# Kernel tuning notes

Measured on AMD Instinct MI355X. Metric: run time of the kernel, lower is better.

The kernel has to match this reference:

```python
import jax, jax.numpy as jnp
import numpy as np

LENGTH = 4096
BATCH = 4096
N_OBS = 2


def setup_inputs() -> dict:
    key = jax.random.key(0)
    k1, k2, k3 = jax.random.split(key, 3)
    # Scale potentials down: the original chain performs no message
    # normalization, so we keep per-step log-growth tiny to avoid overflow.
    j = jax.random.normal(k1, (), dtype=jnp.float32) * 0.01
    b = jax.random.normal(k2, (N_OBS,), dtype=jnp.float32) * 0.01
    observations = jax.random.randint(k3, (BATCH, LENGTH), 0, N_OBS, dtype=jnp.int32)
    return {"j": j, "b": b, "observations": observations}


def reference(j, b, observations):
    # Max-product belief propagation on a binary-state chain CRF,
    # vectorized over the batch and scanned over the chain length.
    B, L = observations.shape
    values = jnp.array([-0.5, 0.5], dtype=jnp.float32)          # states {0,1} - 0.5
    pairs = values[:, None] * values[None, :]                    # [2,2] outer product
    psi = jnp.exp(j * pairs)                                     # [2,2] pairwise potential
    # Unary potentials phi[b_idx, i, s] = exp(b[obs] * values[s])
    phi = jnp.exp(b[observations][..., None] * values)           # [B,L,2]
    phi_tm = jnp.transpose(phi, (1, 0, 2))                       # time-major [L,B,2]

    def step(msg, phi_t):
        # msg_new[k] = max_l phi_t[l] * msg[l] * psi[k,l]
        x = phi_t * msg                                          # [B,2]
        new = jnp.max(x[:, None, :] * psi[None, :, :], axis=2)   # [B,2]
        return new, new

    ones = jnp.ones((B, 2), dtype=phi.dtype)
    # Forward messages: column 0 is ones, column t uses obs[0..t-1]
    _, fwd_msgs = jax.lax.scan(step, ones, phi_tm[:-1])          # [L-1,B,2]
    forward = jnp.concatenate([ones[None], fwd_msgs], axis=0)    # [L,B,2]
    # Backward messages: iterate i = L-1 .. 1, last column is ones
    _, bwd_msgs = jax.lax.scan(step, ones, phi_tm[1:][::-1])     # [L-1,B,2]
    backward = jnp.concatenate([bwd_msgs[::-1], ones[None]], axis=0)  # [L,B,2]

    beliefs = phi_tm * forward * backward                        # [L,B,2]
    return jnp.transpose(beliefs, (1, 2, 0))                     # [B,2,L]
```

## Files before the change

### kernel.cpp

```cpp
#include <hip/hip_runtime.h>
#include <hip/hip_bf16.h>
#include <math.h>

#define LENGTH 4096
#define BATCH  4096
#define CHUNK  8
#define NTHR   512
#define NWAVE  (NTHR / 64)

typedef float vf4 __attribute__((ext_vector_type(4)));

__device__ __forceinline__ void mp_compose(
    float a00, float a01, float a10, float a11,
    float b00, float b01, float b10, float b11,
    float& d00, float& d01, float& d10, float& d11) {
  d00 = fmaxf(a00 + b00, a01 + b10);
  d01 = fmaxf(a00 + b01, a01 + b11);
  d10 = fmaxf(a10 + b00, a11 + b10);
  d11 = fmaxf(a10 + b01, a11 + b11);
}

__device__ __forceinline__ void mp_step(
    float& f00, float& f01, float& f10, float& f11, float ui, float q) {
  float a0l0 = f00 - ui, a1l0 = f10 + ui;
  float a0l1 = f01 - ui, a1l1 = f11 + ui;
  float n00 = fmaxf(a0l0 + q, a1l0 - q);
  float n10 = fmaxf(a0l0 - q, a1l0 + q);
  float n01 = fmaxf(a0l1 + q, a1l1 - q);
  float n11 = fmaxf(a0l1 - q, a1l1 + q);
  f00 = n00; f01 = n01; f10 = n10; f11 = n11;
}

__global__ __launch_bounds__(NTHR, 8) void chain_bp_kernel(
    const float* __restrict__ jp, const float* __restrict__ bp,
    const int* __restrict__ obs, float* __restrict__ out) {
  const int row  = blockIdx.x;
  const int tid  = threadIdx.x;
  const int lane = tid & 63;
  const int wv   = tid >> 6;

  const float j  = jp[0];
  const float q  = 0.25f * j;
  const float u0 = 0.5f * bp[0];
  const float u1 = 0.5f * bp[1];
  const float wb = -fabsf(q);

  const int t0 = tid * CHUNK;
  const int4* op = reinterpret_cast<const int4*>(obs + (size_t)row * LENGTH + t0);
  float u[CHUNK];
#pragma unroll
  for (int v = 0; v < CHUNK / 4; ++v) {
    int4 o = op[v];
    u[4 * v + 0] = o.x ? u1 : u0;
    u[4 * v + 1] = o.y ? u1 : u0;
    u[4 * v + 2] = o.z ? u1 : u0;
    u[4 * v + 3] = o.w ? u1 : u0;
  }

  float l00 = -u[0] + q, l01 = u[0] - q, l10 = -u[0] - q, l11 = u[0] + q;
  float h00 = -u[4] + q, h01 = u[4] - q, h10 = -u[4] - q, h11 = u[4] + q;
#pragma unroll
  for (int i = 1; i < 4; ++i) {
    mp_step(l00, l01, l10, l11, u[i], q);
    mp_step(h00, h01, h10, h11, u[4 + i], q);
  }
  float f00, f01, f10, f11;
  mp_compose(h00, h01, h10, h11, l00, l01, l10, l11, f00, f01, f10, f11);

  float x00 = f00, x01 = f01, x10 = f10, x11 = f11;
#pragma unroll
  for (int d = 1; d < 64; d <<= 1) {
    float p00 = __shfl_up(x00, d), p01 = __shfl_up(x01, d);
    float p10 = __shfl_up(x10, d), p11 = __shfl_up(x11, d);
    if (lane >= d) {
      float n00, n01, n10, n11;
      mp_compose(x00, x01, x10, x11, p00, p01, p10, p11, n00, n01, n10, n11);
      x00 = n00; x01 = n01; x10 = n10; x11 = n11;
    }
  }
  float y00 = f00, y01 = f10, y10 = f01, y11 = f11;
#pragma unroll
  for (int d = 1; d < 64; d <<= 1) {
    float p00 = __shfl_down(y00, d), p01 = __shfl_down(y01, d);
    float p10 = __shfl_down(y10, d), p11 = __shfl_down(y11, d);
    if (lane + d < 64) {
      float n00, n01, n10, n11;
      mp_compose(y00, y01, y10, y11, p00, p01, p10, p11, n00, n01, n10, n11);
      y00 = n00; y01 = n01; y10 = n10; y11 = n11;
    }
  }

  __shared__ float smp[NWAVE][4];
  __shared__ float sms[NWAVE][4];
  if (lane == 63) { smp[wv][0] = x00; smp[wv][1] = x01; smp[wv][2] = x10; smp[wv][3] = x11; }
  if (lane == 0)  { sms[wv][0] = y00; sms[wv][1] = y01; sms[wv][2] = y10; sms[wv][3] = y11; }
  __syncthreads();

  float fh0 = 0.f, fh1 = 0.f;
  for (int k = 0; k < wv; ++k) {
    float m00 = smp[k][0], m01 = smp[k][1], m10 = smp[k][2], m11 = smp[k][3];
    float n0 = fmaxf(m00 + fh0, m01 + fh1);
    float n1 = fmaxf(m10 + fh0, m11 + fh1);
    fh0 = n0; fh1 = n1;
  }
  float wt0 = wb, wt1 = wb;
  for (int k = NWAVE - 1; k > wv; --k) {
    float m00 = sms[k][0], m01 = sms[k][1], m10 = sms[k][2], m11 = sms[k][3];
    float n0 = fmaxf(m00 + wt0, m01 + wt1);
    float n1 = fmaxf(m10 + wt0, m11 + wt1);
    wt0 = n0; wt1 = n1;
  }

  float z0 = fmaxf(x00 + fh0, x01 + fh1);
  float z1 = fmaxf(x10 + fh0, x11 + fh1);
  float zp0 = __shfl_up(z0, 1), zp1 = __shfl_up(z1, 1);
  float fi0 = (lane == 0) ? fh0 : zp0;
  float fi1 = (lane == 0) ? fh1 : zp1;

  float yv0 = fmaxf(y00 + wt0, y01 + wt1);
  float yv1 = fmaxf(y10 + wt0, y11 + wt1);
  float yn0 = __shfl_down(yv0, 1), yn1 = __shfl_down(yv1, 1);
  float wc0 = (lane == 63) ? wt0 : yn0;
  float wc1 = (lane == 63) ? wt1 : yn1;
  float g0 = fmaxf(q + wc0, -q + wc1);
  float g1 = fmaxf(-q + wc0, q + wc1);

  float b0[CHUNK], b1[CHUNK];
  b0[CHUNK - 1] = g0; b1[CHUNK - 1] = g1;
#pragma unroll
  for (int i = CHUNK - 1; i > 0; --i) {
    float ui = u[i];
    float a0 = b0[i] - ui;
    float a1 = b1[i] + ui;
    b0[i - 1] = fmaxf(a0 + q, a1 - q);
    b1[i - 1] = fmaxf(a0 - q, a1 + q);
  }

  float fw0 = fi0, fw1 = fi1;
  vf4 p0lo, p0hi, p1lo, p1hi;
#pragma unroll
  for (int i = 0; i < CHUNK; ++i) {
    float ui = u[i];
    float e0 = __expf(-ui + fw0 + b0[i]);
    float e1 = __expf( ui + fw1 + b1[i]);
    if (i < 4) { p0lo[i] = e0; p1lo[i] = e1; }
    else       { p0hi[i - 4] = e0; p1hi[i - 4] = e1; }
    float a0 = fw0 - ui, a1 = fw1 + ui;
    float n0 = fmaxf(a0 + q, a1 - q);
    float n1 = fmaxf(a0 - q, a1 + q);
    fw0 = n0; fw1 = n1;
  }
  float* outp = out + (size_t)row * (2 * LENGTH) + t0;
  *reinterpret_cast<vf4*>(outp)              = p0lo;
  *reinterpret_cast<vf4*>(outp + 4)          = p0hi;
  *reinterpret_cast<vf4*>(outp + LENGTH)     = p1lo;
  *reinterpret_cast<vf4*>(outp + LENGTH + 4) = p1hi;
}

extern "C" void kernel_launch(void* const* d_in, const int* in_sizes, int n_in,
                              void* d_out, int out_size, void* d_ws, size_t ws_size,
                              hipStream_t stream) {
  const float* jp  = (const float*)d_in[0];
  const float* bp  = (const float*)d_in[1];
  const int*   obs = (const int*)d_in[2];
  float* out = (float*)d_out;

  chain_bp_kernel<<<BATCH, NTHR, 0, stream>>>(jp, bp, obs, out);
}
```

Measured before the change: 190.4 us.

## Build per-block lookup table for 8-step transfer matrices; interleave scans; use exp2

Each block now builds a 256-entry shared-memory table of the composed 8-step max-plus transfer matrices, one per observation pattern. Each thread fetches its chunk matrix by a bit index instead of computing eight steps. The forward and backward wave scans are interleaved in one loop to raise instruction-level parallelism. Log-domain quantities are pre-scaled by log2(e) so the hardware exp2 replaces __expf. The table build costs two extra __syncthreads and some shared memory per block, and the per-thread work it removes is small.

```diff
diff --git a/kernel.cpp b/kernel.cpp
--- a/kernel.cpp
+++ b/kernel.cpp
@@ -1,5 +1,4 @@
 #include <hip/hip_runtime.h>
-#include <hip/hip_bf16.h>
 #include <math.h>
 
 #define LENGTH 4096
@@ -39,59 +38,67 @@
   const int lane = tid & 63;
   const int wv   = tid >> 6;
 
+  const float LOG2E = 1.44269504088896f;
   const float j  = jp[0];
-  const float q  = 0.25f * j;
-  const float u0 = 0.5f * bp[0];
-  const float u1 = 0.5f * bp[1];
+  const float q  = 0.25f * j * LOG2E;
+  const float u0 = 0.5f * bp[0] * LOG2E;
+  const float u1 = 0.5f * bp[1] * LOG2E;
   const float wb = -fabsf(q);
+
+  __shared__ vf4 lut4s[16];
+  __shared__ vf4 lut8[256];
+  __shared__ float smp[NWAVE][4];
+  __shared__ float sms[NWAVE][4];
 
   const int t0 = tid * CHUNK;
   const int4* op = reinterpret_cast<const int4*>(obs + (size_t)row * LENGTH + t0);
+  int4 o0 = op[0], o1 = op[1];
   float u[CHUNK];
+  u[0]=o0.x?u1:u0; u[1]=o0.y?u1:u0; u[2]=o0.z?u1:u0; u[3]=o0.w?u1:u0;
+  u[4]=o1.x?u1:u0; u[5]=o1.y?u1:u0; u[6]=o1.z?u1:u0; u[7]=o1.w?u1:u0;
+  int idx = o0.x | (o0.y<<1) | (o0.z<<2) | (o0.w<<3)
+          | (o1.x<<4) | (o1.y<<5) | (o1.z<<6) | (o1.w<<7);
+
+  if (tid < 16) {
+    float ua = (tid & 1) ? u1 : u0;
+    float f00 = -ua + q, f01 = ua - q, f10 = -ua - q, f11 = ua + q;
 #pragma unroll
-  for (int v = 0; v < CHUNK / 4; ++v) {
-    int4 o = op[v];
-    u[4 * v + 0] = o.x ? u1 : u0;
-    u[4 * v + 1] = o.y ? u1 : u0;
-    u[4 * v + 2] = o.z ? u1 : u0;
-    u[4 * v + 3] = o.w ? u1 : u0;
+    for (int k = 1; k < 4; ++k)
+      mp_step(f00, f01, f10, f11, ((tid >> k) & 1) ? u1 : u0, q);
+    lut4s[tid] = (vf4){f00, f01, f10, f11};
   }
+  __syncthreads();
+  if (tid < 256) {
+    vf4 a = lut4s[tid >> 4], c = lut4s[tid & 15];
+    float d00, d01, d10, d11;
+    mp_compose(a[0], a[1], a[2], a[3], c[0], c[1], c[2], c[3], d00, d01, d10, d11);
+    lut8[tid] = (vf4){d00, d01, d10, d11};
+  }
+  __syncthreads();
 
-  float l00 = -u[0] + q, l01 = u[0] - q, l10 = -u[0] - q, l11 = u[0] + q;
-  float h00 = -u[4] + q, h01 = u[4] - q, h10 = -u[4] - q, h11 = u[4] + q;
-#pragma unroll
-  for (int i = 1; i < 4; ++i) {
-    mp_step(l00, l01, l10, l11, u[i], q);
-    mp_step(h00, h01, h10, h11, u[4 + i], q);
-  }
-  float f00, f01, f10, f11;
-  mp_compose(h00, h01, h10, h11, l00, l01, l10, l11, f00, f01, f10, f11);
+  vf4 Fm = lut8[idx];
+  float f00 = Fm[0], f01 = Fm[1], f10 = Fm[2], f11 = Fm[3];
 
   float x00 = f00, x01 = f01, x10 = f10, x11 = f11;
-#pragma unroll
-  for (int d = 1; d < 64; d <<= 1) {
-    float p00 = __shfl_up(x00, d), p01 = __shfl_up(x01, d);
-    float p10 = __shfl_up(x10, d), p11 = __shfl_up(x11, d);
-    if (lane >= d) {
-      float n00, n01, n10, n11;
-      mp_compose(x00, x01, x10, x11, p00, p01, p10, p11, n00, n01, n10, n11);
-      x00 = n00; x01 = n01; x10 = n10; x11 = n11;
-    }
-  }
   float y00 = f00, y01 = f10, y10 = f01, y11 = f11;
 #pragma unroll
   for (int d = 1; d < 64; d <<= 1) {
-    float p00 = __shfl_down(y00, d), p01 = __shfl_down(y01, d);
-    float p10 = __shfl_down(y10, d), p11 = __shfl_down(y11, d);
+    float px00 = __shfl_up(x00, d), px01 = __shfl_up(x01, d);
+    float px10 = __shfl_up(x10, d), px11 = __shfl_up(x11, d);
+    float py00 = __shfl_down(y00, d), py01 = __shfl_down(y01, d);
+    float py10 = __shfl_down(y10, d), py11 = __shfl_down(y11, d);
+    if (lane >= d) {
+      float n00, n01, n10, n11;
+      mp_compose(x00, x01, x10, x11, px00, px01, px10, px11, n00, n01, n10, n11);
+      x00 = n00; x01 = n01; x10 = n10; x11 = n11;
+    }
     if (lane + d < 64) {
       float n00, n01, n10, n11;
-      mp_compose(y00, y01, y10, y11, p00, p01, p10, p11, n00, n01, n10, n11);
+      mp_compose(y00, y01, y10, y11, py00, py01, py10, py11, n00, n01, n10, n11);
       y00 = n00; y01 = n01; y10 = n10; y11 = n11;
     }
   }
 
-  __shared__ float smp[NWAVE][4];
-  __shared__ float sms[NWAVE][4];
   if (lane == 63) { smp[wv][0] = x00; smp[wv][1] = x01; smp[wv][2] = x10; smp[wv][3] = x11; }
   if (lane == 0)  { sms[wv][0] = y00; sms[wv][1] = y01; sms[wv][2] = y10; sms[wv][3] = y11; }
   __syncthreads();
@@ -141,14 +148,13 @@
 #pragma unroll
   for (int i = 0; i < CHUNK; ++i) {
     float ui = u[i];
-    float e0 = __expf(-ui + fw0 + b0[i]);
-    float e1 = __expf( ui + fw1 + b1[i]);
+    float e0 = __builtin_amdgcn_exp2f(-ui + fw0 + b0[i]);
+    float e1 = __builtin_amdgcn_exp2f( ui + fw1 + b1[i]);
     if (i < 4) { p0lo[i] = e0; p1lo[i] = e1; }
     else       { p0hi[i - 4] = e0; p1hi[i - 4] = e1; }
     float a0 = fw0 - ui, a1 = fw1 + ui;
-    float n0 = fmaxf(a0 + q, a1 - q);
-    float n1 = fmaxf(a0 - q, a1 + q);
-    fw0 = n0; fw1 = n1;
+    fw0 = fmaxf(a0 + q, a1 - q);
+    fw1 = fmaxf(a0 - q, a1 + q);
   }
   float* outp = out + (size_t)row * (2 * LENGTH) + t0;
   *reinterpret_cast<vf4*>(outp)              = p0lo;
```

Result: no change. 189.1 us (-0.7%).
